# Optimization experiments

Hardware: AMD Instinct MI355X
Metric: run time of the kernel (lower is better)

Reference implementation:

```python
import jax, jax.numpy as jnp
import numpy as np

B, L, D = 4, 4096, 1024
H, M = 16, 256
DH = D // H  # 64


def setup_inputs() -> dict:
    key = jax.random.key(0)
    ks = jax.random.split(key, 7)
    s = 1.0 / np.sqrt(D).astype(np.float32)  # keep activations O(1) so exp() stays sane
    x = jax.random.normal(ks[0], (B, L, D), dtype=jnp.float32)
    Wq = jax.random.normal(ks[1], (D, D), dtype=jnp.float32) * s
    Wk = jax.random.normal(ks[2], (D, D), dtype=jnp.float32) * s
    Wv = jax.random.normal(ks[3], (D, D), dtype=jnp.float32) * s
    Wo = jax.random.normal(ks[4], (D, D), dtype=jnp.float32) * s
    bo = jnp.zeros((D,), dtype=jnp.float32)
    omega = jax.random.normal(ks[5], (DH, M), dtype=jnp.float32)
    return {"x": x, "Wq": Wq, "Wk": Wk, "Wv": Wv, "Wo": Wo, "bo": bo, "omega": omega}


def _phi(x, omega):
    # x: (B,H,L,dh) -> positive random features (B,H,L,m)
    scale = DH ** 0.25
    x_s = x / scale
    proj = jnp.einsum('bhld,dm->bhlm', x_s, omega)
    norm_sq = jnp.sum(x_s * x_s, axis=-1, keepdims=True) * 0.5
    return jnp.exp(proj - norm_sq) / (M ** 0.5)


def reference(x, Wq, Wk, Wv, Wo, bo, omega):
    # nn.Linear: y = x @ W.T
    def heads(W):
        return (x @ W.T).reshape(B, L, H, DH).transpose(0, 2, 1, 3)
    Q, K, V = heads(Wq), heads(Wk), heads(Wv)
    Q_feat = _phi(Q, omega)   # (B,H,L,m)
    K_feat = _phi(K, omega)   # (B,H,L,m)
    KV = jnp.einsum('bhlm,bhld->bhmd', K_feat, V)      # (B,H,m,dh)
    out = jnp.einsum('bhlm,bhmd->bhld', Q_feat, KV)    # (B,H,L,dh)
    K_sum = K_feat.sum(axis=2)                          # (B,H,m)
    norm = jnp.einsum('bhlm,bhm->bhl', Q_feat, K_sum)
    norm = jnp.clip(norm, 1e-6, None)[..., None]
    out = out / norm
    out = out.transpose(0, 2, 1, 3).reshape(B, L, D)
    return out @ Wo.T + bo
```

## Files before the change

### kernel.cpp

```cpp
#include <hip/hip_runtime.h>

typedef unsigned short u16;
typedef __attribute__((ext_vector_type(4))) float f32x4;
typedef _Float16 f16x8 __attribute__((ext_vector_type(8)));
typedef __attribute__((ext_vector_type(4))) u16   u16x4;
typedef __attribute__((ext_vector_type(8))) u16   u16x8;

#define DEV static __device__ __forceinline__

constexpr int Ll = 4096;

DEV float h2f(u16 v) { _Float16 h; __builtin_memcpy(&h, &v, 2); return (float)h; }
DEV u16 f2h(float f) { _Float16 h = (_Float16)f; u16 u; __builtin_memcpy(&u, &h, 2); return u; }

DEV f32x4 mfma16h(f16x8 a, f16x8 b, f32x4 c) {
    return __builtin_amdgcn_mfma_f32_16x16x32_f16(a, b, c, 0, 0, 0);
}

#if defined(__has_builtin)
#if __has_builtin(__builtin_amdgcn_global_load_lds)
#define HAS_GLLDS 1
#endif
#endif
#ifndef HAS_GLLDS
#define HAS_GLLDS 0
#endif

#define SBAR()  __builtin_amdgcn_s_barrier()
#define SCHED() __builtin_amdgcn_sched_barrier(0)
#define LGKM0() asm volatile("s_waitcnt lgkmcnt(0)" ::: "memory")

#if HAS_GLLDS
#define STG2(BUF, REG, SRC, ROWBASE, TK, KS)                                         \
  { _Pragma("unroll") for (int u_ = 0; u_ < 2; u_++) {                               \
      int row_ = u_ * 128 + wave * 16 + (lane >> 2);                                 \
      int c_ = lane & 3;                                                             \
      const u16* gp_ = (SRC) + (size_t)((ROWBASE) + row_) * 1024 + (TK) * 64         \
                        + (KS) * 32 + ((c_ ^ ((row_ >> 1) & 3)) * 8);                \
      __builtin_amdgcn_global_load_lds(                                              \
        (const __attribute__((address_space(1))) unsigned int*)gp_,                  \
        (__attribute__((address_space(3))) unsigned int*)(sm + (BUF) * 32768 +       \
          (REG) * 8192 + (u_ * 512 + wave * 64) * 8), 16, 0, 0); } }
#else
#define STG2(BUF, REG, SRC, ROWBASE, TK, KS)                                         \
  { _Pragma("unroll") for (int u_ = 0; u_ < 2; u_++) {                               \
      int row_ = u_ * 128 + wave * 16 + (lane >> 2);                                 \
      int c_ = lane & 3;                                                             \
      const u16* gp_ = (SRC) + (size_t)((ROWBASE) + row_) * 1024 + (TK) * 64         \
                        + (KS) * 32 + ((c_ ^ ((row_ >> 1) & 3)) * 8);                \
      *(u16x8*)(sm + (BUF) * 32768 + (REG) * 8192 + (u_ * 512 + wave * 64 + lane) * 8) \
          = *(const u16x8*)gp_; } }
#endif

#if HAS_GLLDS
#define STGO(BUF, U, SRC, ROWBASE, KK)                                               \
  { int rl_ = wave * 16 + (lane >> 2);                                               \
    int c_ = lane & 3;                                                               \
    int grow_ = (((U) >= 1) ? ((U) - 1) * 128 : 0) + rl_;                            \
    const u16* gp_ = (SRC) + (size_t)((ROWBASE) + grow_) * 1024 + (KK)               \
                     + ((c_ ^ ((rl_ >> 1) & 3)) * 8);                                \
    __builtin_amdgcn_global_load_lds(                                                \
        (const __attribute__((address_space(1))) unsigned int*)gp_,                  \
        (__attribute__((address_space(3))) unsigned int*)(sm + (BUF) * 12288 +       \
            (U) * 4096 + wave * 512), 16, 0, 0); }
#else
#define STGO(BUF, U, SRC, ROWBASE, KK)                                               \
  { int rl_ = wave * 16 + (lane >> 2);                                               \
    int c_ = lane & 3;                                                               \
    int grow_ = (((U) >= 1) ? ((U) - 1) * 128 : 0) + rl_;                            \
    const u16* gp_ = (SRC) + (size_t)((ROWBASE) + grow_) * 1024 + (KK)               \
                     + ((c_ ^ ((rl_ >> 1) & 3)) * 8);                                \
    *(u16x8*)(sm + (BUF) * 12288 + (U) * 4096 + wave * 512 + lane * 8)               \
        = *(const u16x8*)gp_; }
#endif

__global__ __launch_bounds__(256) void k_prep(
    const float* __restrict__ x, const float* __restrict__ Wq, const float* __restrict__ Wk,
    const float* __restrict__ Wv, const float* __restrict__ Wo, const float* __restrict__ om,
    u16* __restrict__ xh, u16* __restrict__ Wc, u16* __restrict__ wtp) {
    int bx = blockIdx.x, tid = threadIdx.x;
    if (bx < 16384) {
        size_t i = ((size_t)bx * 256 + tid) * 4;
        f32x4 v = *(const f32x4*)(x + i);
        u16x4 h;
#pragma unroll
        for (int j = 0; j < 4; j++) h[j] = f2h(v[j]);
        *(u16x4*)(xh + i) = h;
    } else if (bx < 20480) {
        int wsel = (bx - 16384) >> 10;
        const float* src = (wsel == 0) ? Wq : (wsel == 1) ? Wk : (wsel == 2) ? Wv : Wo;
        size_t i = ((size_t)((bx - 16384) & 1023) * 256 + tid) * 4;
        f32x4 v = *(const f32x4*)(src + i);
        u16x4 h;
#pragma unroll
        for (int j = 0; j < 4; j++) h[j] = f2h(v[j]);
        *(u16x4*)(Wc + (size_t)wsel * 1048576 + i) = h;
    } else {
        int i = (bx - 20480) * 256 + tid;
        int m = i >> 6, d = i & 63;
        wtp[i] = f2h(om[d * 256 + m] * 0.35355339059327373f);
    }
}

__global__ __launch_bounds__(512, 1) void k_gemm_qkv(
    const u16* __restrict__ Ax, const u16* __restrict__ Bw,
    u16* __restrict__ QK, u16* __restrict__ Vb) {
    __shared__ __align__(16) u16 sm[65536];
    const int tid = threadIdx.x, wave = tid >> 6, lane = tid & 63;
    const int lr = lane & 15, lkq = lane >> 4;
    const int wr = wave >> 2, wc = wave & 3;
    const int bid = blockIdx.x;
    const int work = (bid & 7) * 96 + (bid >> 3);
    const int m0 = (work / 12) * 256, n0 = (work % 12) * 256;
    const int sec = n0 >> 10;

    const int arow = wr * 128 + lr;
    const int aBase = arow * 32 + ((lkq ^ ((arow >> 1) & 3)) * 8);
    const int brow = wc * 64 + lr;
    const int bBase = 16384 + brow * 32 + ((lkq ^ ((brow >> 1) & 3)) * 8);

    f32x4 acc[8][4];
#pragma unroll
    for (int i = 0; i < 8; i++)
#pragma unroll
        for (int j = 0; j < 4; j++)
#pragma unroll
            for (int r = 0; r < 4; r++) acc[i][j][r] = 0.f;

    STG2(0, 0, Ax, m0, 0, 0)
    STG2(0, 2, Bw, n0, 0, 0)
    STG2(0, 1, Ax, m0, 0, 1)
    STG2(0, 3, Bw, n0, 0, 1)
    asm volatile("s_waitcnt vmcnt(4)" ::: "memory");
    SCHED(); SBAR(); SCHED();

    f16x8 bfr[2][4], afr[4];
    for (int t = 0; t < 16; ++t) {
        const u16* bp = sm + (t & 1) * 32768;
        const int nb = (t + 1) & 1;
        const bool st = t < 15;
#pragma unroll
        for (int f = 0; f < 4; f++) afr[f] = *(const f16x8*)&bp[aBase + f * 512];
#pragma unroll
        for (int j = 0; j < 4; j++) bfr[0][j] = *(const f16x8*)&bp[bBase + j * 512];
        if (st) STG2(nb, 0, Ax, m0, t + 1, 0)
        SBAR(); LGKM0(); SCHED();
        __builtin_amdgcn_s_setprio(1);
#pragma unroll
        for (int i = 0; i < 4; i++)
#pragma unroll
            for (int j = 0; j < 4; j++)
                acc[i][j] = mfma16h(afr[i], bfr[0][j], acc[i][j]);
        __builtin_amdgcn_s_setprio(0);
        SCHED();
        if (st) { asm volatile("s_waitcnt vmcnt(2)" ::: "memory"); }
        else    { asm volatile("s_waitcnt vmcnt(0)" ::: "memory"); }
        SCHED(); SBAR(); SCHED();
#pragma unroll
        for (int f = 0; f < 4; f++) afr[f] = *(const f16x8*)&bp[aBase + 8192 + f * 512];
#pragma unroll
        for (int j = 0; j < 4; j++) bfr[1][j] = *(const f16x8*)&bp[bBase + 8192 + j * 512];
        if (st) STG2(nb, 2, Bw, n0, t + 1, 0)
        SBAR(); LGKM0(); SCHED();
        __builtin_amdgcn_s_setprio(1);
#pragma unroll
        for (int i = 0; i < 4; i++)
#pragma unroll
            for (int j = 0; j < 4; j++)
                acc[i][j] = mfma16h(afr[i], bfr[1][j], acc[i][j]);
        __builtin_amdgcn_s_setprio(0);
        SCHED(); SBAR(); SCHED();
#pragma unroll
        for (int f = 0; f < 4; f++) afr[f] = *(const f16x8*)&bp[aBase + 2048 + f * 512];
        if (st) STG2(nb, 1, Ax, m0, t + 1, 1)
        SBAR(); LGKM0(); SCHED();
        __builtin_amdgcn_s_setprio(1);
#pragma unroll
        for (int i = 0; i < 4; i++)
#pragma unroll
            for (int j = 0; j < 4; j++)
                acc[4 + i][j] = mfma16h(afr[i], bfr[0][j], acc[4 + i][j]);
        __builtin_amdgcn_s_setprio(0);
        SCHED(); SBAR(); SCHED();
#pragma unroll
        for (int f = 0; f < 4; f++) afr[f] = *(const f16x8*)&bp[aBase + 8192 + 2048 + f * 512];
        if (st) STG2(nb, 3, Bw, n0, t + 1, 1)
        SBAR(); LGKM0(); SCHED();
        __builtin_amdgcn_s_setprio(1);
#pragma unroll
        for (int i = 0; i < 4; i++)
#pragma unroll
            for (int j = 0; j < 4; j++)
                acc[4 + i][j] = mfma16h(afr[i], bfr[1][j], acc[4 + i][j]);
        __builtin_amdgcn_s_setprio(0);
        SCHED();
        if (st) { asm volatile("s_waitcnt vmcnt(4)" ::: "memory"); }
        SCHED(); SBAR(); SCHED();
    }

    float* ep = (float*)sm;
    for (int g = 0; g < 8; g++) {
        __syncthreads();
        if (wr == (g >> 2)) {
#pragma unroll
            for (int fi = 0; fi < 2; fi++) {
                int fm = (g & 3) * 2 + fi;
#pragma unroll
                for (int fn = 0; fn < 4; fn++)
#pragma unroll
                    for (int r = 0; r < 4; r++)
                        ep[(fi * 16 + (lane >> 4) * 4 + r) * 264 + wc * 64 + fn * 16 + lr] = acc[fm][fn][r];
            }
        }
        __syncthreads();
        int row = tid >> 4, c0 = (tid & 15) * 16;
        int grow = m0 + g * 32 + row;
        u16x8 h0, h1;
#pragma unroll
        for (int j = 0; j < 8; j++) {
            h0[j] = f2h(ep[row * 264 + c0 + j]);
            h1[j] = f2h(ep[row * 264 + c0 + 8 + j]);
        }
        if (sec < 2) {
            size_t o = (size_t)grow * 2048 + (n0 + c0);
            *(u16x8*)(QK + o) = h0; *(u16x8*)(QK + o + 8) = h1;
        } else {
            size_t o = (size_t)grow * 1024 + (n0 - 2048 + c0);
            *(u16x8*)(Vb + o) = h0; *(u16x8*)(Vb + o + 8) = h1;
        }
    }
}

__global__ __launch_bounds__(512, 2) void k_gemm_out(
    const u16* __restrict__ Ab, const u16* __restrict__ Bw,
    const float* __restrict__ bias, float* __restrict__ outp) {
    __shared__ __align__(16) u16 sm[24576];
    const int tid = threadIdx.x, wave = tid >> 6, lane = tid & 63;
    const int lr = lane & 15, lkq = lane >> 4;
    const int wr = wave >> 2, wc = wave & 3;
    const int bid = blockIdx.x;
    const int work = (bid & 7) * 64 + (bid >> 3);
    const int m0 = (work >> 2) * 128, n0 = (work & 3) * 256;

    int aoff[4], boff[4];
#pragma unroll
    for (int f = 0; f < 4; f++) {
        int row = wr * 64 + f * 16 + lr;
        aoff[f] = row * 32 + ((lkq ^ ((row >> 1) & 3)) * 8);
        int rowb = wc * 64 + f * 16 + lr;
        boff[f] = 4096 + rowb * 32 + ((lkq ^ ((rowb >> 1) & 3)) * 8);
    }

    f32x4 acc[4][4];
#pragma unroll
    for (int i = 0; i < 4; i++)
#pragma unroll
        for (int j = 0; j < 4; j++)
#pragma unroll
            for (int r = 0; r < 4; r++) acc[i][j][r] = 0.f;

    STGO(0, 0, Ab, m0, 0)
    STGO(0, 1, Bw, n0, 0)
    STGO(0, 2, Bw, n0, 0)
    asm volatile("s_waitcnt vmcnt(0)" ::: "memory");
    SCHED(); SBAR(); SCHED();

    int cb = 0;
    for (int t = 0; t < 32; ++t) {
        const u16* buf = sm + cb * 12288;
        f16x8 afr[4], bfr[4];
#pragma unroll
        for (int f = 0; f < 4; f++) {
            afr[f] = *(const f16x8*)&buf[aoff[f]];
            bfr[f] = *(const f16x8*)&buf[boff[f]];
        }
        if (t < 31) {
            int kk = (t + 1) * 32;
            STGO(cb ^ 1, 0, Ab, m0, kk)
            STGO(cb ^ 1, 1, Bw, n0, kk)
            STGO(cb ^ 1, 2, Bw, n0, kk)
        }
        SCHED(); SBAR(); LGKM0(); SCHED();
        __builtin_amdgcn_s_setprio(1);
#pragma unroll
        for (int i = 0; i < 4; i++)
#pragma unroll
            for (int j = 0; j < 4; j++)
                acc[i][j] = mfma16h(afr[i], bfr[j], acc[i][j]);
        __builtin_amdgcn_s_setprio(0);
        SCHED();
        if (t < 31) { asm volatile("s_waitcnt vmcnt(0)" ::: "memory"); }
        SCHED(); SBAR(); SCHED();
        cb ^= 1;
    }

    float* ep = (float*)sm;
    for (int g = 0; g < 4; g++) {
        __syncthreads();
        if (wr == (g >> 1)) {
#pragma unroll
            for (int fi = 0; fi < 2; fi++) {
                int fm = (g & 1) * 2 + fi;
#pragma unroll
                for (int fn = 0; fn < 4; fn++)
#pragma unroll
                    for (int r = 0; r < 4; r++)
                        ep[(fi * 16 + (lane >> 4) * 4 + r) * 264 + wc * 64 + fn * 16 + lr] = acc[fm][fn][r];
            }
        }
        __syncthreads();
        int row = tid >> 4, c0 = (tid & 15) * 16;
        int grow = m0 + g * 32 + row;
        float vv[16];
#pragma unroll
        for (int j = 0; j < 16; j++) vv[j] = ep[row * 264 + c0 + j] + bias[n0 + c0 + j];
#pragma unroll
        for (int p = 0; p < 4; p++) {
            f32x4 tv;
#pragma unroll
            for (int q = 0; q < 4; q++) tv[q] = vv[p * 4 + q];
            *(f32x4*)(outp + (size_t)grow * 1024 + n0 + c0 + p * 4) = tv;
        }
    }
}

__global__ __launch_bounds__(256) void k_phik_kv(
    const u16* __restrict__ QK, const u16* __restrict__ wt,
    const u16* __restrict__ Vb, float* __restrict__ KVacc, float* __restrict__ Ksum) {
    __shared__ __align__(16) u16 sKh[64 * 72];
    __shared__ __align__(16) u16 sVt[64 * 72];
    __shared__ __align__(16) u16 sKfT[256 * 72];
    __shared__ float snsq[64];
    const int tid = threadIdx.x, wave = tid >> 6, lane = tid & 63;
    const int lr = lane & 15, lk = (lane >> 4) * 8;
    const int kc = blockIdx.x, bh = blockIdx.y;
    const int b = bh >> 4, h = bh & 15;

    f16x8 wb[4][2];
#pragma unroll
    for (int fn = 0; fn < 4; fn++)
#pragma unroll
        for (int ks = 0; ks < 2; ks++)
            wb[fn][ks] = *(const f16x8*)(wt + (size_t)(wave * 64 + fn * 16 + lr) * 64 + ks * 32 + lk);

    f32x4 akv[4][4];
#pragma unroll
    for (int i = 0; i < 4; i++)
#pragma unroll
        for (int j = 0; j < 4; j++)
#pragma unroll
            for (int r = 0; r < 4; r++) akv[i][j][r] = 0.f;
    float ksm[4] = {0.f, 0.f, 0.f, 0.f};

    const int rowS = tid >> 2, cS = (tid & 3) * 16;
    size_t gK = ((size_t)(b * Ll + kc * 512 + rowS)) * 2048 + 1024 + h * 64 + cS;
    size_t gV = ((size_t)(b * Ll + kc * 512 + rowS)) * 1024 + h * 64 + cS;
    u16x8 kh0 = *(const u16x8*)(QK + gK);
    u16x8 kh1 = *(const u16x8*)(QK + gK + 8);
    u16x8 vv0 = *(const u16x8*)(Vb + gV);
    u16x8 vv1 = *(const u16x8*)(Vb + gV + 8);

    for (int it = 0; it < 8; it++) {
        __syncthreads();
        {
            *(u16x8*)&sKh[rowS * 72 + cS]     = kh0;
            *(u16x8*)&sKh[rowS * 72 + cS + 8] = kh1;
            float s = 0.f;
#pragma unroll
            for (int j = 0; j < 8; j++) {
                float a = h2f(kh0[j]); s += a * a;
                float c = h2f(kh1[j]); s += c * c;
            }
            s += __shfl_xor(s, 1); s += __shfl_xor(s, 2);
            if ((tid & 3) == 0) snsq[rowS] = s * 0.0625f;
        }
        {
#pragma unroll
            for (int j = 0; j < 8; j++) {
                sVt[(cS + j) * 72 + rowS]     = vv0[j];
                sVt[(cS + 8 + j) * 72 + rowS] = vv1[j];
            }
        }
        __syncthreads();
        if (it < 7) {
            gK += 131072; gV += 65536;
            kh0 = *(const u16x8*)(QK + gK);
            kh1 = *(const u16x8*)(QK + gK + 8);
            vv0 = *(const u16x8*)(Vb + gV);
            vv1 = *(const u16x8*)(Vb + gV + 8);
        }
#pragma unroll
        for (int fm = 0; fm < 4; fm++) {
            f32x4 ap[4];
#pragma unroll
            for (int fn = 0; fn < 4; fn++)
#pragma unroll
                for (int r = 0; r < 4; r++) ap[fn][r] = 0.f;
            __builtin_amdgcn_s_setprio(1);
#pragma unroll
            for (int ks = 0; ks < 2; ks++) {
                f16x8 aH = *(const f16x8*)&sKh[(fm * 16 + lr) * 72 + ks * 32 + lk];
#pragma unroll
                for (int fn = 0; fn < 4; fn++)
                    ap[fn] = mfma16h(aH, wb[fn][ks], ap[fn]);
            }
            __builtin_amdgcn_s_setprio(0);
#pragma unroll
            for (int fn = 0; fn < 4; fn++) {
                u16x4 pk;
#pragma unroll
                for (int r = 0; r < 4; r++) {
                    float ns = snsq[fm * 16 + (lane >> 4) * 4 + r];
                    float val = __expf(ap[fn][r] - ns) * 0.00390625f;
                    ksm[fn] += val;
                    pk[r] = f2h(val);
                }
                *(u16x4*)&sKfT[(wave * 64 + fn * 16 + lr) * 72 + fm * 16 + (lane >> 4) * 4] = pk;
            }
        }
        __builtin_amdgcn_s_setprio(1);
#pragma unroll
        for (int ks = 0; ks < 2; ks++) {
            f16x8 a4[4], b4[4];
#pragma unroll
            for (int f = 0; f < 4; f++) {
                a4[f] = *(const f16x8*)&sKfT[(wave * 64 + f * 16 + lr) * 72 + ks * 32 + lk];
                b4[f] = *(const f16x8*)&sVt[(f * 16 + lr) * 72 + ks * 32 + lk];
            }
#pragma unroll
            for (int fm = 0; fm < 4; fm++)
#pragma unroll
                for (int fn = 0; fn < 4; fn++)
                    akv[fm][fn] = mfma16h(a4[fm], b4[fn], akv[fm][fn]);
        }
        __builtin_amdgcn_s_setprio(0);
    }
    const size_t base = ((size_t)(kc * 64 + bh)) << 14;
#pragma unroll
    for (int fm = 0; fm < 4; fm++)
#pragma unroll
        for (int fn = 0; fn < 4; fn++)
#pragma unroll
            for (int r = 0; r < 4; r++) {
                int m = wave * 64 + fm * 16 + (lane >> 4) * 4 + r;
                int d = fn * 16 + lr;
                KVacc[base + m * 64 + d] = akv[fm][fn][r];
            }
#pragma unroll
    for (int fn = 0; fn < 4; fn++) {
        ksm[fn] += __shfl_xor(ksm[fn], 16);
        ksm[fn] += __shfl_xor(ksm[fn], 32);
    }
    if (lane < 16) {
#pragma unroll
        for (int fn = 0; fn < 4; fn++)
            Ksum[(kc * 64 + bh) * 256 + wave * 64 + fn * 16 + lane] = ksm[fn];
    }
}

__global__ __launch_bounds__(256) void k_kvt(const float* __restrict__ KVacc,
                                             const float* __restrict__ Ksum,
                                             u16* __restrict__ KVt, float* __restrict__ KsumR) {
    int i = blockIdx.x * 256 + threadIdx.x;
    if (blockIdx.x < 16384) {
        int bh = i >> 14, m = (i >> 6) & 255, d = i & 63;
        float s = 0.f;
#pragma unroll
        for (int kc = 0; kc < 8; kc++)
            s += KVacc[(((size_t)(kc * 64 + bh)) << 14) + m * 64 + d];
        KVt[((size_t)bh << 14) + d * 256 + m] = f2h(s);
    } else {
        int j = i - 4194304;
        int bh = j >> 8, m = j & 255;
        float s = 0.f;
#pragma unroll
        for (int kc = 0; kc < 8; kc++)
            s += Ksum[(kc * 64 + bh) * 256 + m];
        KsumR[j] = s;
    }
}

__global__ __launch_bounds__(512) void k_phiq_attn(
    const u16* __restrict__ QK, const u16* __restrict__ wt,
    const u16* __restrict__ KVt, const float* __restrict__ Ksum,
    u16* __restrict__ attn) {
    __shared__ __align__(16) u16 sQh[64 * 72];
    __shared__ __align__(16) u16 sQf[64 * 264];
    __shared__ float sKs[256];
    __shared__ float snsq[64];
    __shared__ float snorm[64];
    const int tid = threadIdx.x, wave = tid >> 6, lane = tid & 63;
    const int lr = lane & 15, lk = (lane >> 4) * 8;
    const int bh = blockIdx.y, b = bh >> 4, h = bh & 15;
    const int mq = wave & 3;
    const int lh = wave >> 2;
    const int af = wave & 3;
    const int ad = wave >> 2;

    f16x8 wb[4][2];
#pragma unroll
    for (int fn = 0; fn < 4; fn++)
#pragma unroll
        for (int ks = 0; ks < 2; ks++)
            wb[fn][ks] = *(const f16x8*)(wt + (size_t)(mq * 64 + fn * 16 + lr) * 64 + ks * 32 + lk);
    f16x8 kvb[2][8];
#pragma unroll
    for (int fn = 0; fn < 2; fn++)
#pragma unroll
        for (int ks = 0; ks < 8; ks++)
            kvb[fn][ks] = *(const f16x8*)(KVt + ((size_t)bh << 14) +
                                          (size_t)(ad * 32 + fn * 16 + lr) * 256 + ks * 32 + lk);
    if (tid < 256) sKs[tid] = Ksum[bh * 256 + tid];

    const int rowQ = tid >> 3, cQ = (tid & 7) * 8;
    size_t gQ = ((size_t)(b * Ll + blockIdx.x * 256 + rowQ)) * 2048 + h * 64 + cQ;
    u16x8 vh = *(const u16x8*)(QK + gQ);

    for (int st = 0; st < 4; st++) {
        const int l0 = blockIdx.x * 256 + st * 64;
        __syncthreads();
        {
            *(u16x8*)&sQh[rowQ * 72 + cQ] = vh;
            float s = 0.f;
#pragma unroll
            for (int j = 0; j < 8; j++) { float a = h2f(vh[j]); s += a * a; }
            s += __shfl_xor(s, 1); s += __shfl_xor(s, 2); s += __shfl_xor(s, 4);
            if ((tid & 7) == 0) snsq[rowQ] = s * 0.0625f;
        }
        __syncthreads();
#pragma unroll
        for (int fm = 0; fm < 2; fm++) {
            f32x4 ap[4];
#pragma unroll
            for (int fn = 0; fn < 4; fn++)
#pragma unroll
                for (int r = 0; r < 4; r++) ap[fn][r] = 0.f;
            __builtin_amdgcn_s_setprio(1);
#pragma unroll
            for (int ks = 0; ks < 2; ks++) {
                f16x8 aH = *(const f16x8*)&sQh[(lh * 32 + fm * 16 + lr) * 72 + ks * 32 + lk];
#pragma unroll
                for (int fn = 0; fn < 4; fn++)
                    ap[fn] = mfma16h(aH, wb[fn][ks], ap[fn]);
            }
            __builtin_amdgcn_s_setprio(0);
#pragma unroll
            for (int fn = 0; fn < 4; fn++)
#pragma unroll
                for (int r = 0; r < 4; r++) {
                    int l = lh * 32 + fm * 16 + (lane >> 4) * 4 + r;
                    int m = mq * 64 + fn * 16 + lr;
                    sQf[l * 264 + m] = f2h(__expf(ap[fn][r] - snsq[l]) * 0.0625f);
                }
        }
        if (st < 3) {
            gQ += 131072;
            vh = *(const u16x8*)(QK + gQ);
        }
        __syncthreads();
        {
            int l = tid >> 3, m0 = (tid & 7) * 32;
            float s = 0.f;
#pragma unroll
            for (int j4 = 0; j4 < 4; j4++) {
                u16x8 qv = *(const u16x8*)&sQf[l * 264 + m0 + j4 * 8];
#pragma unroll
                for (int j = 0; j < 8; j++) s += h2f(qv[j]) * sKs[m0 + j4 * 8 + j];
            }
            s += __shfl_xor(s, 1); s += __shfl_xor(s, 2); s += __shfl_xor(s, 4);
            if ((tid & 7) == 0) snorm[l] = s;
        }
        f32x4 aa[2];
#pragma unroll
        for (int fn = 0; fn < 2; fn++)
#pragma unroll
            for (int r = 0; r < 4; r++) aa[fn][r] = 0.f;
        __builtin_amdgcn_s_setprio(1);
#pragma unroll
        for (int ks = 0; ks < 8; ks++) {
            f16x8 a = *(const f16x8*)&sQf[(af * 16 + lr) * 264 + ks * 32 + lk];
            aa[0] = mfma16h(a, kvb[0][ks], aa[0]);
            aa[1] = mfma16h(a, kvb[1][ks], aa[1]);
        }
        __builtin_amdgcn_s_setprio(0);
        __syncthreads();
        float* ep = (float*)sQf;
#pragma unroll
        for (int fn = 0; fn < 2; fn++)
#pragma unroll
            for (int r = 0; r < 4; r++) {
                int l = af * 16 + (lane >> 4) * 4 + r;
                int d = ad * 32 + fn * 16 + lr;
                ep[l * 68 + d] = aa[fn][r];
            }
        __syncthreads();
        {
            int l = tid >> 3, d0 = (tid & 7) * 8;
            float inv = 1.0f / fmaxf(snorm[l], 6.25e-8f);
            u16x8 o;
#pragma unroll
            for (int j = 0; j < 8; j++) o[j] = f2h(ep[l * 68 + d0 + j] * inv);
            *(u16x8*)(attn + ((size_t)(b * Ll + l0 + l)) * 1024 + h * 64 + d0) = o;
        }
    }
}

extern "C" void kernel_launch(void* const* d_in, const int* in_sizes, int n_in,
                              void* d_out, int out_size, void* d_ws, size_t ws_size,
                              hipStream_t stream) {
    (void)in_sizes; (void)n_in; (void)out_size; (void)ws_size;
    const float* x  = (const float*)d_in[0];
    const float* Wq = (const float*)d_in[1];
    const float* Wk = (const float*)d_in[2];
    const float* Wv = (const float*)d_in[3];
    const float* Wo = (const float*)d_in[4];
    const float* bo = (const float*)d_in[5];
    const float* om = (const float*)d_in[6];

    char* w = (char*)d_ws;
    size_t o = 0;
    auto take = [&](size_t n) { char* p = w + o; o += n; return p; };
    u16* QK  = (u16*)take(67108864);
    u16* Vb  = (u16*)take(33554432);
    u16* xh  = (u16*)take(33554432);
    u16* Wc  = (u16*)take(8388608);
    u16* wt  = (u16*)take(32768);
    float* KVacc = (float*)take(33554432);
    float* Ksum  = (float*)take(524288);
    float* KsumR = (float*)take(65536);
    u16* KVt = (u16*)take(2097152);
    u16* Wof  = Wc + 3145728;
    u16* attn = Vb;

    k_prep<<<20544, 256, 0, stream>>>(x, Wq, Wk, Wv, Wo, om, xh, Wc, wt);
    k_gemm_qkv<<<768, 512, 0, stream>>>(xh, Wc, QK, Vb);
    k_phik_kv<<<dim3(8, 64), 256, 0, stream>>>(QK, wt, Vb, KVacc, Ksum);
    k_kvt<<<16448, 256, 0, stream>>>(KVacc, Ksum, KVt, KsumR);
    k_phiq_attn<<<dim3(16, 64), 512, 0, stream>>>(QK, wt, KVt, KsumR, attn);
    k_gemm_out<<<512, 512, 0, stream>>>(attn, Wof, bo, (float*)d_out);
}
```

Baseline: 360.0 us.

## Restructure QKV GEMM LDS staging to full 64-wide rows with 8-way XOR swizzle

The QKV projection GEMM now stages each K-tile as full 64-element rows, one 128-byte row per eight lanes, using an 8-way XOR swizzle instead of two separate 32-wide halves. All eight global-to-LDS loads for the next tile are issued at the top of the iteration, and the wait for them moves to a single vmcnt(0) at the end. The aim is wider, more coalesced global reads, fewer LDS bank conflicts, and simpler wait accounting. The cost is a burst of loads issued at once, with less interleaving of loads across the four MFMA phases.

```diff
diff --git a/kernel.cpp b/kernel.cpp
--- a/kernel.cpp
+++ b/kernel.cpp
@@ -31,25 +31,21 @@
 #define LGKM0() asm volatile("s_waitcnt lgkmcnt(0)" ::: "memory")
 
 #if HAS_GLLDS
-#define STG2(BUF, REG, SRC, ROWBASE, TK, KS)                                         \
-  { _Pragma("unroll") for (int u_ = 0; u_ < 2; u_++) {                               \
-      int row_ = u_ * 128 + wave * 16 + (lane >> 2);                                 \
-      int c_ = lane & 3;                                                             \
-      const u16* gp_ = (SRC) + (size_t)((ROWBASE) + row_) * 1024 + (TK) * 64         \
-                        + (KS) * 32 + ((c_ ^ ((row_ >> 1) & 3)) * 8);                \
-      __builtin_amdgcn_global_load_lds(                                              \
-        (const __attribute__((address_space(1))) unsigned int*)gp_,                  \
-        (__attribute__((address_space(3))) unsigned int*)(sm + (BUF) * 32768 +       \
-          (REG) * 8192 + (u_ * 512 + wave * 64) * 8), 16, 0, 0); } }
+#define STG3(BUF, TB, J, SRC, ROWBASE, TK)                                           \
+  { int row_ = (J) * 64 + wave * 8 + (lane >> 3);                                    \
+    int cg_ = (lane & 7) ^ ((lane >> 3) & 7);                                        \
+    const u16* gp_ = (SRC) + (size_t)((ROWBASE) + row_) * 1024 + (TK) * 64 + cg_ * 8;\
+    __builtin_amdgcn_global_load_lds(                                                \
+      (const __attribute__((address_space(1))) unsigned int*)gp_,                    \
+      (__attribute__((address_space(3))) unsigned int*)(sm + (BUF) * 32768 +         \
+        (TB) + (J) * 4096 + wave * 512), 16, 0, 0); }
 #else
-#define STG2(BUF, REG, SRC, ROWBASE, TK, KS)                                         \
-  { _Pragma("unroll") for (int u_ = 0; u_ < 2; u_++) {                               \
-      int row_ = u_ * 128 + wave * 16 + (lane >> 2);                                 \
-      int c_ = lane & 3;                                                             \
-      const u16* gp_ = (SRC) + (size_t)((ROWBASE) + row_) * 1024 + (TK) * 64         \
-                        + (KS) * 32 + ((c_ ^ ((row_ >> 1) & 3)) * 8);                \
-      *(u16x8*)(sm + (BUF) * 32768 + (REG) * 8192 + (u_ * 512 + wave * 64 + lane) * 8) \
-          = *(const u16x8*)gp_; } }
+#define STG3(BUF, TB, J, SRC, ROWBASE, TK)                                           \
+  { int row_ = (J) * 64 + wave * 8 + (lane >> 3);                                    \
+    int cg_ = (lane & 7) ^ ((lane >> 3) & 7);                                        \
+    const u16* gp_ = (SRC) + (size_t)((ROWBASE) + row_) * 1024 + (TK) * 64 + cg_ * 8;\
+    *(u16x8*)(sm + (BUF) * 32768 + (TB) + (J) * 4096 + wave * 512 + lane * 8)        \
+        = *(const u16x8*)gp_; }
 #endif
 
 #if HAS_GLLDS
@@ -114,10 +110,11 @@
     const int m0 = (work / 12) * 256, n0 = (work % 12) * 256;
     const int sec = n0 >> 10;
 
-    const int arow = wr * 128 + lr;
-    const int aBase = arow * 32 + ((lkq ^ ((arow >> 1) & 3)) * 8);
-    const int brow = wc * 64 + lr;
-    const int bBase = 16384 + brow * 32 + ((lkq ^ ((brow >> 1) & 3)) * 8);
+    const int e = lr & 7;
+    const int aB0 = (wr * 128 + lr) * 64 + ((lkq ^ e) * 8);
+    const int aB1 = aB0 ^ 32;
+    const int bB0 = 16384 + (wc * 64 + lr) * 64 + ((lkq ^ e) * 8);
+    const int bB1 = bB0 ^ 32;
 
     f32x4 acc[8][4];
 #pragma unroll
@@ -127,11 +124,11 @@
 #pragma unroll
             for (int r = 0; r < 4; r++) acc[i][j][r] = 0.f;
 
-    STG2(0, 0, Ax, m0, 0, 0)
-    STG2(0, 2, Bw, n0, 0, 0)
-    STG2(0, 1, Ax, m0, 0, 1)
-    STG2(0, 3, Bw, n0, 0, 1)
-    asm volatile("s_waitcnt vmcnt(4)" ::: "memory");
+    STG3(0, 0,     0, Ax, m0, 0) STG3(0, 0,     1, Ax, m0, 0)
+    STG3(0, 0,     2, Ax, m0, 0) STG3(0, 0,     3, Ax, m0, 0)
+    STG3(0, 16384, 0, Bw, n0, 0) STG3(0, 16384, 1, Bw, n0, 0)
+    STG3(0, 16384, 2, Bw, n0, 0) STG3(0, 16384, 3, Bw, n0, 0)
+    asm volatile("s_waitcnt vmcnt(0)" ::: "memory");
     SCHED(); SBAR(); SCHED();
 
     f16x8 bfr[2][4], afr[4];
@@ -140,10 +137,15 @@
         const int nb = (t + 1) & 1;
         const bool st = t < 15;
 #pragma unroll
-        for (int f = 0; f < 4; f++) afr[f] = *(const f16x8*)&bp[aBase + f * 512];
-#pragma unroll
-        for (int j = 0; j < 4; j++) bfr[0][j] = *(const f16x8*)&bp[bBase + j * 512];
-        if (st) STG2(nb, 0, Ax, m0, t + 1, 0)
+        for (int f = 0; f < 4; f++) afr[f] = *(const f16x8*)&bp[aB0 + f * 1024];
+#pragma unroll
+        for (int j = 0; j < 4; j++) bfr[0][j] = *(const f16x8*)&bp[bB0 + j * 1024];
+        if (st) {
+            STG3(nb, 0,     0, Ax, m0, t + 1) STG3(nb, 0,     1, Ax, m0, t + 1)
+            STG3(nb, 0,     2, Ax, m0, t + 1) STG3(nb, 0,     3, Ax, m0, t + 1)
+            STG3(nb, 16384, 0, Bw, n0, t + 1) STG3(nb, 16384, 1, Bw, n0, t + 1)
+            STG3(nb, 16384, 2, Bw, n0, t + 1) STG3(nb, 16384, 3, Bw, n0, t + 1)
+        }
         SBAR(); LGKM0(); SCHED();
         __builtin_amdgcn_s_setprio(1);
 #pragma unroll
@@ -152,15 +154,11 @@
             for (int j = 0; j < 4; j++)
                 acc[i][j] = mfma16h(afr[i], bfr[0][j], acc[i][j]);
         __builtin_amdgcn_s_setprio(0);
-        SCHED();
-        if (st) { asm volatile("s_waitcnt vmcnt(2)" ::: "memory"); }
-        else    { asm volatile("s_waitcnt vmcnt(0)" ::: "memory"); }
         SCHED(); SBAR(); SCHED();
 #pragma unroll
-        for (int f = 0; f < 4; f++) afr[f] = *(const f16x8*)&bp[aBase + 8192 + f * 512];
-#pragma unroll
-        for (int j = 0; j < 4; j++) bfr[1][j] = *(const f16x8*)&bp[bBase + 8192 + j * 512];
-        if (st) STG2(nb, 2, Bw, n0, t + 1, 0)
+        for (int f = 0; f < 4; f++) afr[f] = *(const f16x8*)&bp[aB1 + f * 1024];
+#pragma unroll
+        for (int j = 0; j < 4; j++) bfr[1][j] = *(const f16x8*)&bp[bB1 + j * 1024];
         SBAR(); LGKM0(); SCHED();
         __builtin_amdgcn_s_setprio(1);
 #pragma unroll
@@ -171,8 +169,7 @@
         __builtin_amdgcn_s_setprio(0);
         SCHED(); SBAR(); SCHED();
 #pragma unroll
-        for (int f = 0; f < 4; f++) afr[f] = *(const f16x8*)&bp[aBase + 2048 + f * 512];
-        if (st) STG2(nb, 1, Ax, m0, t + 1, 1)
+        for (int f = 0; f < 4; f++) afr[f] = *(const f16x8*)&bp[aB0 + 4096 + f * 1024];
         SBAR(); LGKM0(); SCHED();
         __builtin_amdgcn_s_setprio(1);
 #pragma unroll
@@ -183,8 +180,7 @@
         __builtin_amdgcn_s_setprio(0);
         SCHED(); SBAR(); SCHED();
 #pragma unroll
-        for (int f = 0; f < 4; f++) afr[f] = *(const f16x8*)&bp[aBase + 8192 + 2048 + f * 512];
-        if (st) STG2(nb, 3, Bw, n0, t + 1, 1)
+        for (int f = 0; f < 4; f++) afr[f] = *(const f16x8*)&bp[aB1 + 4096 + f * 1024];
         SBAR(); LGKM0(); SCHED();
         __builtin_amdgcn_s_setprio(1);
 #pragma unroll
@@ -194,7 +190,7 @@
                 acc[4 + i][j] = mfma16h(afr[i], bfr[1][j], acc[4 + i][j]);
         __builtin_amdgcn_s_setprio(0);
         SCHED();
-        if (st) { asm volatile("s_waitcnt vmcnt(4)" ::: "memory"); }
+        if (st) { asm volatile("s_waitcnt vmcnt(0)" ::: "memory"); }
         SCHED(); SBAR(); SCHED();
     }
 
```

After: 358.6 us. No clear change (-0.4%).
